# Performance work log

Hardware: AMD Instinct MI355X
Metric: run time of the kernel (lower is better)

## Reference

```python
import jax, jax.numpy as jnp
import numpy as np

VOCAB = 100000
EMB = 100
HID = 100
CTX_LEN = 60          # must equal MAX_DESC_LEN for linear_1 to fit
FACT_LEN = 20
DESC_LEN = 60


def setup_inputs() -> dict:
    key = jax.random.key(0)
    ks = jax.random.split(key, 12)
    s = 0.05
    context = jax.random.randint(ks[0], (CTX_LEN, FACT_LEN), 1, VOCAB)
    fact_lengths = jax.random.randint(ks[1], (CTX_LEN,), 1, FACT_LEN)
    description = jax.random.randint(ks[2], (DESC_LEN,), 1, VOCAB)
    emb_ctx = jax.random.normal(ks[3], (VOCAB, EMB), jnp.float32) * s
    emb_ctx = emb_ctx.at[0].set(0.0)  # padding_idx=0
    emb_dec = jax.random.normal(ks[4], (VOCAB, EMB), jnp.float32) * s
    emb_dec = emb_dec.at[0].set(0.0)
    w1 = jax.random.normal(ks[5], (HID, CTX_LEN * HID), jnp.float32) * s
    b1 = jax.random.normal(ks[6], (HID,), jnp.float32) * s
    w_ih = jax.random.normal(ks[7], (3 * HID, EMB), jnp.float32) * s
    w_hh = jax.random.normal(ks[8], (3 * HID, HID), jnp.float32) * s
    b_ih = jax.random.normal(ks[9], (3 * HID,), jnp.float32) * s
    b_hh = jax.random.normal(ks[10], (3 * HID,), jnp.float32) * s
    w_out = jax.random.normal(ks[11], (VOCAB, HID), jnp.float32) * s
    b_out = jnp.zeros((VOCAB,), jnp.float32)
    return {"context": context, "fact_lengths": fact_lengths, "description": description,
            "emb_ctx": emb_ctx, "emb_dec": emb_dec, "w1": w1, "b1": b1,
            "w_ih": w_ih, "w_hh": w_hh, "b_ih": b_ih, "b_hh": b_hh,
            "w_out": w_out, "b_out": b_out}


def _forward(context, description, emb_ctx, emb_dec, w1, b1,
             w_ih, w_hh, b_ih, b_hh, w_out, b_out):
    # ---- InputModule: embed + positional fact encoder ----
    emb = emb_ctx[context]                       # [CTX_LEN, FACT_LEN, EMB]
    slen, elen = FACT_LEN, EMB
    s = jnp.arange(slen, dtype=jnp.float32) / (slen - 1)   # [slen]
    e = jnp.arange(elen, dtype=jnp.float32) / (elen - 1)   # [elen]
    l = 1.0 - s[:, None] - e[None, :] * (1.0 - 2.0 * s[:, None])  # [slen, elen]
    facts = jnp.sum(emb * l[None], axis=1)       # [CTX_LEN, EMB]

    # ---- initial decoder hidden from flattened facts ----
    h0 = facts.reshape(1, -1) @ w1.T + b1        # [1, HID]

    x0 = emb_dec[1][None, :]                     # SOS token embedding [1, EMB]

    def step(carry, tok):
        h, x = carry
        gi = x @ w_ih.T + b_ih                   # [1, 3H]
        gh = h @ w_hh.T + b_hh
        i_r, i_z, i_n = jnp.split(gi, 3, axis=-1)
        h_r, h_z, h_n = jnp.split(gh, 3, axis=-1)
        r = jax.nn.sigmoid(i_r + h_r)
        z = jax.nn.sigmoid(i_z + h_z)
        n = jnp.tanh(i_n + r * h_n)
        h_new = (1.0 - z) * n + z * h            # [1, HID]
        logits = h_new @ w_out.T + b_out         # [1, VOCAB]
        logp = jax.nn.log_softmax(logits, axis=-1)
        loss_t = -logp[0, tok]                   # NLLLoss, batch 1
        x_next = emb_dec[tok][None, :]           # teacher forcing
        return (h_new, x_next), loss_t

    (_, _), losses = jax.lax.scan(step, (h0, x0), description)
    return jnp.sum(losses).reshape(1)            # matches torch FloatTensor([.])


def reference(context, fact_lengths, description, emb_ctx, emb_dec, w1, b1,
              w_ih, w_hh, b_ih, b_hh, w_out, b_out):
    # fact_lengths is unused by the original forward (PositionalFactEncoder ignores it)
    return _forward(context, description, emb_ctx, emb_dec, w1, b1,
                    w_ih, w_hh, b_ih, b_hh, w_out, b_out)
```

## Files before the change

### kernel.cpp

```cpp
#include <hip/hip_runtime.h>
#include <hip/hip_bf16.h>
#include <math.h>

#define VOCAB 100000
#define EMB 100
#define HID 100
#define CTX_LEN 60
#define FACT_LEN 20
#define DESC_LEN 60
#define NCHUNK (VOCAB / 16)

#define WS_FACTS 0
#define WS_X     6000
#define WS_H0    12000
#define WS_GI    12160
#define WS_H     30160
#define WS_MS    36864
#define WS_WBF   1048576

typedef __attribute__((ext_vector_type(8))) short short8;
typedef __attribute__((ext_vector_type(4))) float f32x4;

static __device__ __forceinline__ unsigned short f2bf(float f) {
    union { float f; unsigned u; } x; x.f = f;
    unsigned r = (x.u + 0x7FFFu + ((x.u >> 16) & 1u)) >> 16;
    return (unsigned short)r;
}

__global__ __launch_bounds__(128) void k1_prep(const int* __restrict__ context,
                                               const int* __restrict__ desc,
                                               const float* __restrict__ emb_ctx,
                                               const float* __restrict__ emb_dec,
                                               float* __restrict__ ws,
                                               float* __restrict__ out) {
    int b = blockIdx.x, tid = threadIdx.x;
    if (b < 60) {
        __shared__ int toks[20];
        if (tid < 20) toks[tid] = context[b * 20 + tid];
        __syncthreads();
        if (tid < 100) {
            float ef = tid * (1.f / 99.f);
            float acc = 0.f;
            #pragma unroll
            for (int s = 0; s < 20; s++) {
                float sf = s * (1.f / 19.f);
                float l = 1.f - sf - ef * (1.f - 2.f * sf);
                acc = fmaf(emb_ctx[toks[s] * 100 + tid], l, acc);
            }
            ws[WS_FACTS + b * 100 + tid] = acc;
        }
    } else {
        int t = b - 60;
        int tok = (t == 0) ? 1 : desc[t - 1];
        if (tid < 100) ws[WS_X + t * 100 + tid] = emb_dec[tok * 100 + tid];
        if (b == 60 && tid == 0) out[0] = 0.f;
    }
}

__global__ __launch_bounds__(320) void k2_h0_gi(const float* __restrict__ w1,
                                                const float* __restrict__ b1,
                                                const float* __restrict__ w_ih,
                                                const float* __restrict__ b_ih,
                                                float* __restrict__ ws) {
    int b = blockIdx.x, tid = threadIdx.x;
    if (b < 100) {
        __shared__ float red[320];
        const float* facts = ws + WS_FACTS;
        const float* wr = w1 + b * 6000;
        float p = 0.f;
        for (int k = tid; k < 6000; k += 320) p = fmaf(facts[k], wr[k], p);
        red[tid] = p; __syncthreads();
        if (tid < 64) red[tid] += red[256 + tid];
        __syncthreads();
        for (int st = 128; st > 0; st >>= 1) {
            if (tid < st) red[tid] += red[tid + st];
            __syncthreads();
        }
        if (tid == 0) ws[WS_H0 + b] = red[0] + b1[b];
    } else {
        int t = b - 100;
        __shared__ float xs[100];
        if (tid < 100) xs[tid] = ws[WS_X + t * 100 + tid];
        __syncthreads();
        if (tid < 300) {
            float p = b_ih[tid];
            const float* wr = w_ih + tid * 100;
            #pragma unroll 4
            for (int k = 0; k < 100; k++) p = fmaf(wr[k], xs[k], p);
            ws[WS_GI + t * 300 + tid] = p;
        }
    }
}

__global__ __launch_bounds__(320, 1) void k3_gru_cvt(const float* __restrict__ w_hh,
                                                     const float* __restrict__ b_hh,
                                                     const float* __restrict__ w_out,
                                                     float* __restrict__ ws) {
    if (blockIdx.x != 0) {
        const int bid = blockIdx.x - 1;
        unsigned short* wbf = (unsigned short*)((char*)ws + WS_WBF * 4);
        uint2* out4 = (uint2*)wbf;
        const int total = VOCAB * 128 / 4;
        const int stride = 255 * 320;
        for (int i = bid * 320 + threadIdx.x; i < total; i += stride) {
            int row = i >> 5;
            int k0 = (i & 31) * 4;
            uint2 r;
            if (k0 + 4 <= 100) {
                float4 v = *(const float4*)(w_out + row * 100 + k0);
                r.x = (unsigned)f2bf(v.x) | ((unsigned)f2bf(v.y) << 16);
                r.y = (unsigned)f2bf(v.z) | ((unsigned)f2bf(v.w) << 16);
            } else { r.x = 0u; r.y = 0u; }
            out4[i] = r;
        }
        return;
    }

    __shared__ __align__(16) float gi_lds[18000];
    __shared__ __align__(16) float h_hist[6000];
    __shared__ __align__(16) unsigned short h_bf[128];

    const int tid = threadIdx.x;
    const int wave = tid >> 6, lane = tid & 63;
    const int q = lane >> 4, n = lane & 15;
    const int l = lane;
    const int j = 20 * wave + l;

    short8 bfr[16];
    #pragma unroll
    for (int i = 0; i < 4; i++) {
        int row;
        if (i == 0)      row = 20 * wave + n;
        else if (i == 1) row = 100 + 20 * wave + n;
        else if (i == 2) row = 200 + 20 * wave + n;
        else {
            if (n < 4)       row = 20 * wave + 16 + n;
            else if (n < 8)  row = 100 + 20 * wave + 12 + n;
            else if (n < 12) row = 200 + 20 * wave + 8 + n;
            else             row = -1;
        }
        const float* wr = w_hh + (row < 0 ? 0 : row) * 100;
        #pragma unroll
        for (int kt = 0; kt < 4; kt++) {
            int k0 = kt * 32 + q * 8;
            float va[8];
            #pragma unroll
            for (int jj = 0; jj < 8; jj++) va[jj] = 0.f;
            if (row >= 0) {
                if (k0 + 4 <= 100) {
                    float4 a = *(const float4*)(wr + k0);
                    va[0] = a.x; va[1] = a.y; va[2] = a.z; va[3] = a.w;
                }
                if (k0 + 8 <= 100) {
                    float4 b = *(const float4*)(wr + k0 + 4);
                    va[4] = b.x; va[5] = b.y; va[6] = b.z; va[7] = b.w;
                }
            }
            short8 f;
            #pragma unroll
            for (int jj = 0; jj < 8; jj++) f[jj] = (short)f2bf(va[jj]);
            bfr[i * 4 + kt] = f;
        }
    }

    {
        const float4* g4 = (const float4*)(ws + WS_GI);
        float4* l4 = (float4*)gi_lds;
        for (int k = tid; k < 4500; k += 320) l4[k] = g4[k];
    }

    float hreg = 0.f, bh0 = 0.f, bh1 = 0.f, bh2 = 0.f;
    if (l < 20) {
        hreg = ws[WS_H0 + j];
        bh0 = b_hh[j]; bh1 = b_hh[100 + j]; bh2 = b_hh[200 + j];
        h_bf[j] = f2bf(hreg);
    }
    if (tid >= 100 && tid < 128) h_bf[tid] = 0;
    __syncthreads();

    const int s_lo  = (l < 16) ? l : 0;
    const int s3r   = (l < 16) ? 0 : (l - 16);
    const int s3z   = (l < 16) ? 4 : (l - 12);
    const int s3n   = (l < 16) ? 8 : (l - 8);

    for (int t = 0; t < 60; t++) {
        short8 afr[4];
        #pragma unroll
        for (int kt = 0; kt < 4; kt++)
            afr[kt] = *(const short8*)&h_bf[kt * 32 + q * 8];

        float val[4];
        #pragma unroll
        for (int i = 0; i < 4; i++) {
            f32x4 z4 = {0.f, 0.f, 0.f, 0.f};
            f32x4 a01 = __builtin_amdgcn_mfma_f32_16x16x32_bf16(afr[0], bfr[i * 4 + 0], z4, 0, 0, 0);
            a01 = __builtin_amdgcn_mfma_f32_16x16x32_bf16(afr[1], bfr[i * 4 + 1], a01, 0, 0, 0);
            f32x4 a23 = __builtin_amdgcn_mfma_f32_16x16x32_bf16(afr[2], bfr[i * 4 + 2], z4, 0, 0, 0);
            a23 = __builtin_amdgcn_mfma_f32_16x16x32_bf16(afr[3], bfr[i * 4 + 3], a23, 0, 0, 0);
            val[i] = a01[0] + a23[0];
        }

        float v0  = __shfl(val[0], s_lo, 64);
        float v1  = __shfl(val[1], s_lo, 64);
        float v2  = __shfl(val[2], s_lo, 64);
        float w3r = __shfl(val[3], s3r, 64);
        float w3z = __shfl(val[3], s3z, 64);
        float w3n = __shfl(val[3], s3n, 64);

        if (l < 20) {
            float ghr = ((l < 16) ? v0 : w3r) + bh0;
            float ghz = ((l < 16) ? v1 : w3z) + bh1;
            float ghn = ((l < 16) ? v2 : w3n) + bh2;
            float gir = gi_lds[t * 300 + j];
            float giz = gi_lds[t * 300 + 100 + j];
            float gin = gi_lds[t * 300 + 200 + j];
            float r = 1.f / (1.f + __expf(-(gir + ghr)));
            float z = 1.f / (1.f + __expf(-(giz + ghz)));
            float a = fmaf(r, ghn, gin);
            float tt = __expf(-2.f * fabsf(a));
            float nn = copysignf((1.f - tt) / (1.f + tt), a);
            hreg = (1.f - z) * nn + z * hreg;
            h_bf[j] = f2bf(hreg);
            h_hist[t * 100 + j] = hreg;
        }
        __syncthreads();
    }

    {
        float4* Hg = (float4*)(ws + WS_H);
        const float4* h4 = (const float4*)h_hist;
        for (int k = tid; k < 1500; k += 320) Hg[k] = h4[k];
    }
}

__global__ __launch_bounds__(256, 1) void k4_logits(const float* __restrict__ b_out,
                                                    float* __restrict__ ws,
                                                    int nwaves) {
    const float* H = ws + WS_H;
    const unsigned short* wbf = (const unsigned short*)((const char*)ws + WS_WBF * 4);
    float* ms = ws + WS_MS;
    const int lane = threadIdx.x & 63;
    const int gw = blockIdx.x * 4 + (threadIdx.x >> 6);
    const int q = lane >> 4, n = lane & 15;
    const int k_base = q * 8;

    short8 afr[4][4];
    #pragma unroll
    for (int mt = 0; mt < 4; mt++) {
        int m = mt * 16 + n;
        #pragma unroll
        for (int kt = 0; kt < 4; kt++) {
            int k0 = kt * 32 + k_base;
            float va[8];
            #pragma unroll
            for (int jj = 0; jj < 8; jj++) va[jj] = 0.f;
            if (m < 60) {
                if (k0 + 4 <= 100) {
                    float4 a = *(const float4*)(H + m * 100 + k0);
                    va[0] = a.x; va[1] = a.y; va[2] = a.z; va[3] = a.w;
                }
                if (k0 + 8 <= 100) {
                    float4 b = *(const float4*)(H + m * 100 + k0 + 4);
                    va[4] = b.x; va[5] = b.y; va[6] = b.z; va[7] = b.w;
                }
            }
            short8 f;
            #pragma unroll
            for (int jj = 0; jj < 8; jj++) f[jj] = (short)f2bf(va[jj]);
            afr[mt][kt] = f;
        }
    }

    float mS[16], sS[16];
    #pragma unroll
    for (int i = 0; i < 16; i++) { mS[i] = -3.0e38f; sS[i] = 0.f; }

    for (int c = gw; c < NCHUNK; c += nwaves) {
        int row = c * 16 + n;
        const short8* bp = (const short8*)(wbf + (size_t)row * 128);
        short8 bfr[4];
        #pragma unroll
        for (int kt = 0; kt < 4; kt++) bfr[kt] = bp[kt * 4 + q];
        float bo = b_out[row];
        #pragma unroll
        for (int mt = 0; mt < 4; mt++) {
            f32x4 acc = {0.f, 0.f, 0.f, 0.f};
            acc = __builtin_amdgcn_mfma_f32_16x16x32_bf16(afr[mt][0], bfr[0], acc, 0, 0, 0);
            acc = __builtin_amdgcn_mfma_f32_16x16x32_bf16(afr[mt][1], bfr[1], acc, 0, 0, 0);
            acc = __builtin_amdgcn_mfma_f32_16x16x32_bf16(afr[mt][2], bfr[2], acc, 0, 0, 0);
            acc = __builtin_amdgcn_mfma_f32_16x16x32_bf16(afr[mt][3], bfr[3], acc, 0, 0, 0);
            #pragma unroll
            for (int reg = 0; reg < 4; reg++) {
                float x = acc[reg] + bo;
                int i = mt * 4 + reg;
                float mo = mS[i];
                float mn = fmaxf(mo, x);
                sS[i] = sS[i] * __expf(mo - mn) + __expf(x - mn);
                mS[i] = mn;
            }
        }
    }

    #pragma unroll
    for (int i = 0; i < 16; i++) {
        float m = mS[i], s = sS[i];
        #pragma unroll
        for (int off = 1; off < 16; off <<= 1) {
            float m2 = __shfl_xor(m, off);
            float s2 = __shfl_xor(s, off);
            float mn = fmaxf(m, m2);
            s = s * __expf(m - mn) + s2 * __expf(m2 - mn);
            m = mn;
        }
        mS[i] = m; sS[i] = s;
    }
    if (n == 0) {
        #pragma unroll
        for (int mt = 0; mt < 4; mt++) {
            #pragma unroll
            for (int reg = 0; reg < 4; reg++) {
                int t = mt * 16 + q * 4 + reg;
                int i = mt * 4 + reg;
                if (t < 60) {
                    float2 val; val.x = mS[i]; val.y = sS[i];
                    ((float2*)ms)[t * nwaves + gw] = val;
                }
            }
        }
    }
}

__global__ __launch_bounds__(256) void k5_final(const int* __restrict__ desc,
                                                const float* __restrict__ w_out,
                                                const float* __restrict__ b_out,
                                                const float* __restrict__ ws,
                                                float* __restrict__ out,
                                                int nwaves) {
    int t = blockIdx.x, tid = threadIdx.x;
    __shared__ float sm[256], ss[256], sd[256];
    const float2* ms = (const float2*)(ws + WS_MS);
    float m = -3.0e38f, s = 0.f;
    for (int i = tid; i < nwaves; i += 256) {
        float2 p = ms[t * nwaves + i];
        float mn = fmaxf(m, p.x);
        s = s * __expf(m - mn) + p.y * __expf(p.x - mn);
        m = mn;
    }
    sm[tid] = m; ss[tid] = s; __syncthreads();
    for (int st = 128; st > 0; st >>= 1) {
        if (tid < st) {
            float mo = sm[tid], so = ss[tid];
            float m2 = sm[tid + st], s2 = ss[tid + st];
            float mn = fmaxf(mo, m2);
            sm[tid] = mn;
            ss[tid] = so * __expf(mo - mn) + s2 * __expf(m2 - mn);
        }
        __syncthreads();
    }
    int tok = desc[t];
    float p = 0.f;
    if (tid < 100) p = ws[WS_H + t * 100 + tid] * w_out[tok * 100 + tid];
    sd[tid] = p; __syncthreads();
    for (int st = 128; st > 0; st >>= 1) {
        if (tid < st) sd[tid] += sd[tid + st];
        __syncthreads();
    }
    if (tid == 0) {
        float logit = sd[0] + b_out[tok];
        float loss = sm[0] + logf(ss[0]) - logit;
        atomicAdd(out, loss);
    }
}

extern "C" void kernel_launch(void* const* d_in, const int* in_sizes, int n_in,
                              void* d_out, int out_size, void* d_ws, size_t ws_size,
                              hipStream_t stream) {
    const int*   context = (const int*)d_in[0];
    const int*   desc    = (const int*)d_in[2];
    const float* emb_ctx = (const float*)d_in[3];
    const float* emb_dec = (const float*)d_in[4];
    const float* w1      = (const float*)d_in[5];
    const float* b1      = (const float*)d_in[6];
    const float* w_ih    = (const float*)d_in[7];
    const float* w_hh    = (const float*)d_in[8];
    const float* b_ih    = (const float*)d_in[9];
    const float* b_hh    = (const float*)d_in[10];
    const float* w_out   = (const float*)d_in[11];
    const float* b_out   = (const float*)d_in[12];
    float* out = (float*)d_out;
    float* ws  = (float*)d_ws;

    int nblocks = 1024;
    size_t need = (size_t)(WS_WBF) * 4 + (size_t)VOCAB * 128 * 2;
    size_t need_ms = (size_t)(WS_MS + 60 * (nblocks * 4) * 2) * 4;
    if (need_ms > need) need = need_ms;
    if (ws_size < need) nblocks = 256;
    int nwaves = nblocks * 4;

    k1_prep   <<<120, 128, 0, stream>>>(context, desc, emb_ctx, emb_dec, ws, out);
    k2_h0_gi  <<<160, 320, 0, stream>>>(w1, b1, w_ih, b_ih, ws);
    k3_gru_cvt<<<256, 320, 0, stream>>>(w_hh, b_hh, w_out, ws);
    k4_logits <<<nblocks, 256, 0, stream>>>(b_out, ws, nwaves);
    k5_final  <<<60,  256, 0, stream>>>(desc, w_out, b_out, ws, out, nwaves);
}
```

Before: 211.5 us.

## Fuse GRU, logits and loss into one persistent kernel with flag sync

Merges the GRU, bf16 weight-conversion, logits/log-sum-exp and final-loss kernels into a single persistent kernel. The worker blocks convert w_out, spin on a global flag set by the GRU block, then compute partial softmax statistics. The last block to finish, detected with an atomic counter, does the final reduction. Target-logit dot products move into the GRU block, and the decoder embedding gather is folded into the input-gate kernel, removing two launches and intermediate traffic. In exchange it depends on all 256 blocks being co-resident and on the workspace flags starting at a 0xAA fill pattern on every call, which is fragile.

```diff
diff --git a/kernel.cpp b/kernel.cpp
--- a/kernel.cpp
+++ b/kernel.cpp
@@ -9,12 +9,16 @@
 #define FACT_LEN 20
 #define DESC_LEN 60
 #define NCHUNK (VOCAB / 16)
+#define NWLOG  1275
+#define MSSTRIDE 1280
 
 #define WS_FACTS 0
-#define WS_X     6000
 #define WS_H0    12000
 #define WS_GI    12160
 #define WS_H     30160
+#define WS_LT    36400
+#define WS_FLAGH 36600
+#define WS_FLAGD 36632
 #define WS_MS    36864
 #define WS_WBF   1048576
 
@@ -27,33 +31,23 @@
     return (unsigned short)r;
 }
 
-__global__ __launch_bounds__(128) void k1_prep(const int* __restrict__ context,
-                                               const int* __restrict__ desc,
-                                               const float* __restrict__ emb_ctx,
-                                               const float* __restrict__ emb_dec,
-                                               float* __restrict__ ws,
-                                               float* __restrict__ out) {
+__global__ __launch_bounds__(128) void k1_facts(const int* __restrict__ context,
+                                                const float* __restrict__ emb_ctx,
+                                                float* __restrict__ ws) {
     int b = blockIdx.x, tid = threadIdx.x;
-    if (b < 60) {
-        __shared__ int toks[20];
-        if (tid < 20) toks[tid] = context[b * 20 + tid];
-        __syncthreads();
-        if (tid < 100) {
-            float ef = tid * (1.f / 99.f);
-            float acc = 0.f;
-            #pragma unroll
-            for (int s = 0; s < 20; s++) {
-                float sf = s * (1.f / 19.f);
-                float l = 1.f - sf - ef * (1.f - 2.f * sf);
-                acc = fmaf(emb_ctx[toks[s] * 100 + tid], l, acc);
-            }
-            ws[WS_FACTS + b * 100 + tid] = acc;
-        }
-    } else {
-        int t = b - 60;
-        int tok = (t == 0) ? 1 : desc[t - 1];
-        if (tid < 100) ws[WS_X + t * 100 + tid] = emb_dec[tok * 100 + tid];
-        if (b == 60 && tid == 0) out[0] = 0.f;
+    __shared__ int toks[20];
+    if (tid < 20) toks[tid] = context[b * 20 + tid];
+    __syncthreads();
+    if (tid < 100) {
+        float ef = tid * (1.f / 99.f);
+        float acc = 0.f;
+        #pragma unroll
+        for (int s = 0; s < 20; s++) {
+            float sf = s * (1.f / 19.f);
+            float l = 1.f - sf - ef * (1.f - 2.f * sf);
+            acc = fmaf(emb_ctx[toks[s] * 100 + tid], l, acc);
+        }
+        ws[WS_FACTS + b * 100 + tid] = acc;
     }
 }
 
@@ -61,6 +55,8 @@
                                                 const float* __restrict__ b1,
                                                 const float* __restrict__ w_ih,
                                                 const float* __restrict__ b_ih,
+                                                const int* __restrict__ desc,
+                                                const float* __restrict__ emb_dec,
                                                 float* __restrict__ ws) {
     int b = blockIdx.x, tid = threadIdx.x;
     if (b < 100) {
@@ -80,7 +76,10 @@
     } else {
         int t = b - 100;
         __shared__ float xs[100];
-        if (tid < 100) xs[tid] = ws[WS_X + t * 100 + tid];
+        __shared__ int tok_s;
+        if (tid == 0) tok_s = (t == 0) ? 1 : desc[t - 1];
+        __syncthreads();
+        if (tid < 100) xs[tid] = emb_dec[tok_s * 100 + tid];
         __syncthreads();
         if (tid < 300) {
             float p = b_ih[tid];
@@ -92,37 +91,183 @@
     }
 }
 
-__global__ __launch_bounds__(320, 1) void k3_gru_cvt(const float* __restrict__ w_hh,
-                                                     const float* __restrict__ b_hh,
-                                                     const float* __restrict__ w_out,
-                                                     float* __restrict__ ws) {
-    if (blockIdx.x != 0) {
-        const int bid = blockIdx.x - 1;
-        unsigned short* wbf = (unsigned short*)((char*)ws + WS_WBF * 4);
-        uint2* out4 = (uint2*)wbf;
-        const int total = VOCAB * 128 / 4;
-        const int stride = 255 * 320;
-        for (int i = bid * 320 + threadIdx.x; i < total; i += stride) {
-            int row = i >> 5;
-            int k0 = (i & 31) * 4;
-            uint2 r;
-            if (k0 + 4 <= 100) {
-                float4 v = *(const float4*)(w_out + row * 100 + k0);
-                r.x = (unsigned)f2bf(v.x) | ((unsigned)f2bf(v.y) << 16);
-                r.y = (unsigned)f2bf(v.z) | ((unsigned)f2bf(v.w) << 16);
-            } else { r.x = 0u; r.y = 0u; }
-            out4[i] = r;
-        }
-        return;
-    }
-
+__global__ __launch_bounds__(320, 1) void k3_mega(const float* __restrict__ w_hh,
+                                                  const float* __restrict__ b_hh,
+                                                  const float* __restrict__ w_out,
+                                                  const float* __restrict__ b_out,
+                                                  const int* __restrict__ desc,
+                                                  float* __restrict__ ws,
+                                                  float* __restrict__ out) {
     __shared__ __align__(16) float gi_lds[18000];
     __shared__ __align__(16) float h_hist[6000];
     __shared__ __align__(16) unsigned short h_bf[128];
+    __shared__ float loss_t[64];
+    __shared__ unsigned lds_last;
 
     const int tid = threadIdx.x;
     const int wave = tid >> 6, lane = tid & 63;
     const int q = lane >> 4, n = lane & 15;
+    unsigned* flagH = (unsigned*)(ws + WS_FLAGH);
+    unsigned* flagD = (unsigned*)(ws + WS_FLAGD);
+
+    if (blockIdx.x != 0) {
+        const int bid = blockIdx.x - 1;
+        unsigned short* wbf = (unsigned short*)(ws + WS_WBF);
+        {
+            uint2* out4 = (uint2*)wbf;
+            const int total = VOCAB * 128 / 4;
+            const int stride = 255 * 320;
+            for (int i = bid * 320 + tid; i < total; i += stride) {
+                int row = i >> 5;
+                int k0 = (i & 31) * 4;
+                uint2 r;
+                if (k0 + 4 <= 100) {
+                    float4 v = *(const float4*)(w_out + row * 100 + k0);
+                    r.x = (unsigned)f2bf(v.x) | ((unsigned)f2bf(v.y) << 16);
+                    r.y = (unsigned)f2bf(v.z) | ((unsigned)f2bf(v.w) << 16);
+                } else { r.x = 0u; r.y = 0u; }
+                out4[i] = r;
+            }
+        }
+        if (tid == 0) {
+            unsigned v;
+            do {
+                v = atomicAdd(flagH, 0u);
+                if (v != 1u) __builtin_amdgcn_s_sleep(16);
+            } while (v != 1u);
+        }
+        __syncthreads();
+        __threadfence();
+
+        const float* H = ws + WS_H;
+        float* ms = ws + WS_MS;
+        const int gw = bid * 5 + wave;
+        const int k_base = q * 8;
+
+        short8 afr[4][4];
+        #pragma unroll
+        for (int mt = 0; mt < 4; mt++) {
+            int m = mt * 16 + n;
+            #pragma unroll
+            for (int kt = 0; kt < 4; kt++) {
+                int k0 = kt * 32 + k_base;
+                float va[8];
+                #pragma unroll
+                for (int jj = 0; jj < 8; jj++) va[jj] = 0.f;
+                if (m < 60) {
+                    if (k0 + 4 <= 100) {
+                        float4 a = *(const float4*)(H + m * 100 + k0);
+                        va[0] = a.x; va[1] = a.y; va[2] = a.z; va[3] = a.w;
+                    }
+                    if (k0 + 8 <= 100) {
+                        float4 b = *(const float4*)(H + m * 100 + k0 + 4);
+                        va[4] = b.x; va[5] = b.y; va[6] = b.z; va[7] = b.w;
+                    }
+                }
+                short8 f;
+                #pragma unroll
+                for (int jj = 0; jj < 8; jj++) f[jj] = (short)f2bf(va[jj]);
+                afr[mt][kt] = f;
+            }
+        }
+
+        float mS[16], sS[16];
+        #pragma unroll
+        for (int i = 0; i < 16; i++) { mS[i] = -3.0e38f; sS[i] = 0.f; }
+
+        for (int c = gw; c < NCHUNK; c += NWLOG) {
+            int row = c * 16 + n;
+            const short8* bp = (const short8*)(wbf + (size_t)row * 128);
+            short8 bfr[4];
+            #pragma unroll
+            for (int kt = 0; kt < 4; kt++) bfr[kt] = bp[kt * 4 + q];
+            float bo = b_out[row];
+            #pragma unroll
+            for (int mt = 0; mt < 4; mt++) {
+                f32x4 acc = {0.f, 0.f, 0.f, 0.f};
+                acc = __builtin_amdgcn_mfma_f32_16x16x32_bf16(afr[mt][0], bfr[0], acc, 0, 0, 0);
+                acc = __builtin_amdgcn_mfma_f32_16x16x32_bf16(afr[mt][1], bfr[1], acc, 0, 0, 0);
+                acc = __builtin_amdgcn_mfma_f32_16x16x32_bf16(afr[mt][2], bfr[2], acc, 0, 0, 0);
+                acc = __builtin_amdgcn_mfma_f32_16x16x32_bf16(afr[mt][3], bfr[3], acc, 0, 0, 0);
+                #pragma unroll
+                for (int reg = 0; reg < 4; reg++) {
+                    float x = acc[reg] + bo;
+                    int i = mt * 4 + reg;
+                    float mo = mS[i];
+                    float mn = fmaxf(mo, x);
+                    sS[i] = sS[i] * __expf(mo - mn) + __expf(x - mn);
+                    mS[i] = mn;
+                }
+            }
+        }
+
+        #pragma unroll
+        for (int i = 0; i < 16; i++) {
+            float m = mS[i], s = sS[i];
+            #pragma unroll
+            for (int off = 1; off < 16; off <<= 1) {
+                float m2 = __shfl_xor(m, off);
+                float s2 = __shfl_xor(s, off);
+                float mn = fmaxf(m, m2);
+                s = s * __expf(m - mn) + s2 * __expf(m2 - mn);
+                m = mn;
+            }
+            mS[i] = m; sS[i] = s;
+        }
+        if (n == 0) {
+            #pragma unroll
+            for (int mt = 0; mt < 4; mt++) {
+                #pragma unroll
+                for (int reg = 0; reg < 4; reg++) {
+                    int t = mt * 16 + q * 4 + reg;
+                    if (t < 60) {
+                        int i = mt * 4 + reg;
+                        float2 val; val.x = mS[i]; val.y = sS[i];
+                        ((float2*)ms)[t * MSSTRIDE + gw] = val;
+                    }
+                }
+            }
+        }
+
+        __threadfence();
+        __syncthreads();
+        if (tid == 0) {
+            unsigned old = atomicAdd(flagD, 1u);
+            lds_last = (old == 0xAAAAAAAAu + 254u) ? 1u : 0u;
+        }
+        __syncthreads();
+        if (lds_last) {
+            __threadfence();
+            const float2* msp = (const float2*)(ws + WS_MS);
+            for (int tt = 0; tt < 12; tt++) {
+                int t = wave * 12 + tt;
+                float m = -3.0e38f, s = 0.f;
+                for (int i = lane; i < NWLOG; i += 64) {
+                    float2 p = msp[t * MSSTRIDE + i];
+                    float mn = fmaxf(m, p.x);
+                    s = s * __expf(m - mn) + p.y * __expf(p.x - mn);
+                    m = mn;
+                }
+                #pragma unroll
+                for (int off = 1; off < 64; off <<= 1) {
+                    float m2 = __shfl_xor(m, off);
+                    float s2 = __shfl_xor(s, off);
+                    float mn = fmaxf(m, m2);
+                    s = s * __expf(m - mn) + s2 * __expf(m2 - mn);
+                    m = mn;
+                }
+                if (lane == 0) loss_t[t] = m + logf(s) - ws[WS_LT + t];
+            }
+            __syncthreads();
+            if (tid == 0) {
+                float tot = 0.f;
+                for (int t = 0; t < 60; t++) tot += loss_t[t];
+                out[0] = tot;
+            }
+        }
+        return;
+    }
+
     const int l = lane;
     const int j = 20 * wave + l;
 
@@ -231,145 +376,24 @@
         const float4* h4 = (const float4*)h_hist;
         for (int k = tid; k < 1500; k += 320) Hg[k] = h4[k];
     }
-}
-
-__global__ __launch_bounds__(256, 1) void k4_logits(const float* __restrict__ b_out,
-                                                    float* __restrict__ ws,
-                                                    int nwaves) {
-    const float* H = ws + WS_H;
-    const unsigned short* wbf = (const unsigned short*)((const char*)ws + WS_WBF * 4);
-    float* ms = ws + WS_MS;
-    const int lane = threadIdx.x & 63;
-    const int gw = blockIdx.x * 4 + (threadIdx.x >> 6);
-    const int q = lane >> 4, n = lane & 15;
-    const int k_base = q * 8;
-
-    short8 afr[4][4];
-    #pragma unroll
-    for (int mt = 0; mt < 4; mt++) {
-        int m = mt * 16 + n;
-        #pragma unroll
-        for (int kt = 0; kt < 4; kt++) {
-            int k0 = kt * 32 + k_base;
-            float va[8];
-            #pragma unroll
-            for (int jj = 0; jj < 8; jj++) va[jj] = 0.f;
-            if (m < 60) {
-                if (k0 + 4 <= 100) {
-                    float4 a = *(const float4*)(H + m * 100 + k0);
-                    va[0] = a.x; va[1] = a.y; va[2] = a.z; va[3] = a.w;
-                }
-                if (k0 + 8 <= 100) {
-                    float4 b = *(const float4*)(H + m * 100 + k0 + 4);
-                    va[4] = b.x; va[5] = b.y; va[6] = b.z; va[7] = b.w;
-                }
-            }
-            short8 f;
-            #pragma unroll
-            for (int jj = 0; jj < 8; jj++) f[jj] = (short)f2bf(va[jj]);
-            afr[mt][kt] = f;
-        }
-    }
-
-    float mS[16], sS[16];
-    #pragma unroll
-    for (int i = 0; i < 16; i++) { mS[i] = -3.0e38f; sS[i] = 0.f; }
-
-    for (int c = gw; c < NCHUNK; c += nwaves) {
-        int row = c * 16 + n;
-        const short8* bp = (const short8*)(wbf + (size_t)row * 128);
-        short8 bfr[4];
-        #pragma unroll
-        for (int kt = 0; kt < 4; kt++) bfr[kt] = bp[kt * 4 + q];
-        float bo = b_out[row];
-        #pragma unroll
-        for (int mt = 0; mt < 4; mt++) {
-            f32x4 acc = {0.f, 0.f, 0.f, 0.f};
-            acc = __builtin_amdgcn_mfma_f32_16x16x32_bf16(afr[mt][0], bfr[0], acc, 0, 0, 0);
-            acc = __builtin_amdgcn_mfma_f32_16x16x32_bf16(afr[mt][1], bfr[1], acc, 0, 0, 0);
-            acc = __builtin_amdgcn_mfma_f32_16x16x32_bf16(afr[mt][2], bfr[2], acc, 0, 0, 0);
-            acc = __builtin_amdgcn_mfma_f32_16x16x32_bf16(afr[mt][3], bfr[3], acc, 0, 0, 0);
-            #pragma unroll
-            for (int reg = 0; reg < 4; reg++) {
-                float x = acc[reg] + bo;
-                int i = mt * 4 + reg;
-                float mo = mS[i];
-                float mn = fmaxf(mo, x);
-                sS[i] = sS[i] * __expf(mo - mn) + __expf(x - mn);
-                mS[i] = mn;
-            }
-        }
-    }
-
-    #pragma unroll
-    for (int i = 0; i < 16; i++) {
-        float m = mS[i], s = sS[i];
-        #pragma unroll
-        for (int off = 1; off < 16; off <<= 1) {
-            float m2 = __shfl_xor(m, off);
-            float s2 = __shfl_xor(s, off);
-            float mn = fmaxf(m, m2);
-            s = s * __expf(m - mn) + s2 * __expf(m2 - mn);
-            m = mn;
-        }
-        mS[i] = m; sS[i] = s;
-    }
-    if (n == 0) {
-        #pragma unroll
-        for (int mt = 0; mt < 4; mt++) {
-            #pragma unroll
-            for (int reg = 0; reg < 4; reg++) {
-                int t = mt * 16 + q * 4 + reg;
-                int i = mt * 4 + reg;
-                if (t < 60) {
-                    float2 val; val.x = mS[i]; val.y = sS[i];
-                    ((float2*)ms)[t * nwaves + gw] = val;
-                }
-            }
-        }
-    }
-}
-
-__global__ __launch_bounds__(256) void k5_final(const int* __restrict__ desc,
-                                                const float* __restrict__ w_out,
-                                                const float* __restrict__ b_out,
-                                                const float* __restrict__ ws,
-                                                float* __restrict__ out,
-                                                int nwaves) {
-    int t = blockIdx.x, tid = threadIdx.x;
-    __shared__ float sm[256], ss[256], sd[256];
-    const float2* ms = (const float2*)(ws + WS_MS);
-    float m = -3.0e38f, s = 0.f;
-    for (int i = tid; i < nwaves; i += 256) {
-        float2 p = ms[t * nwaves + i];
-        float mn = fmaxf(m, p.x);
-        s = s * __expf(m - mn) + p.y * __expf(p.x - mn);
-        m = mn;
-    }
-    sm[tid] = m; ss[tid] = s; __syncthreads();
-    for (int st = 128; st > 0; st >>= 1) {
-        if (tid < st) {
-            float mo = sm[tid], so = ss[tid];
-            float m2 = sm[tid + st], s2 = ss[tid + st];
-            float mn = fmaxf(mo, m2);
-            sm[tid] = mn;
-            ss[tid] = so * __expf(mo - mn) + s2 * __expf(m2 - mn);
-        }
-        __syncthreads();
-    }
-    int tok = desc[t];
-    float p = 0.f;
-    if (tid < 100) p = ws[WS_H + t * 100 + tid] * w_out[tok * 100 + tid];
-    sd[tid] = p; __syncthreads();
-    for (int st = 128; st > 0; st >>= 1) {
-        if (tid < st) sd[tid] += sd[tid + st];
-        __syncthreads();
-    }
-    if (tid == 0) {
-        float logit = sd[0] + b_out[tok];
-        float loss = sm[0] + logf(ss[0]) - logit;
-        atomicAdd(out, loss);
-    }
+
+    for (int tt = 0; tt < 12; tt++) {
+        int t = wave * 12 + tt;
+        int tok = desc[t];
+        const float* wr = w_out + (size_t)tok * 100;
+        float p = 0.f;
+        if (l < 50) {
+            p = h_hist[t * 100 + 2 * l] * wr[2 * l]
+              + h_hist[t * 100 + 2 * l + 1] * wr[2 * l + 1];
+        }
+        #pragma unroll
+        for (int off = 1; off < 64; off <<= 1) p += __shfl_xor(p, off);
+        if (l == 0) ws[WS_LT + t] = p + b_out[tok];
+    }
+
+    __threadfence();
+    __syncthreads();
+    if (tid == 0) atomicExch(flagH, 1u);
 }
 
 extern "C" void kernel_launch(void* const* d_in, const int* in_sizes, int n_in,
@@ -390,16 +414,7 @@
     float* out = (float*)d_out;
     float* ws  = (float*)d_ws;
 
-    int nblocks = 1024;
-    size_t need = (size_t)(WS_WBF) * 4 + (size_t)VOCAB * 128 * 2;
-    size_t need_ms = (size_t)(WS_MS + 60 * (nblocks * 4) * 2) * 4;
-    if (need_ms > need) need = need_ms;
-    if (ws_size < need) nblocks = 256;
-    int nwaves = nblocks * 4;
-
-    k1_prep   <<<120, 128, 0, stream>>>(context, desc, emb_ctx, emb_dec, ws, out);
-    k2_h0_gi  <<<160, 320, 0, stream>>>(w1, b1, w_ih, b_ih, ws);
-    k3_gru_cvt<<<256, 320, 0, stream>>>(w_hh, b_hh, w_out, ws);
-    k4_logits <<<nblocks, 256, 0, stream>>>(b_out, ws, nwaves);
-    k5_final  <<<60,  256, 0, stream>>>(desc, w_out, b_out, ws, out, nwaves);
+    k1_facts<<<60,  128, 0, stream>>>(context, emb_ctx, ws);
+    k2_h0_gi<<<160, 320, 0, stream>>>(w1, b1, w_ih, b_ih, desc, emb_dec, ws);
+    k3_mega <<<256, 320, 0, stream>>>(w_hh, b_hh, w_out, b_out, desc, ws, out);
 }
```

Measured after the change: 343.5 us. 62.4% more time.
